# Performance work log

Hardware: AMD Instinct MI355X
Metric: run time of the kernel (lower is better)

The kernel has to match this reference:

```python
import jax, jax.numpy as jnp
import numpy as np

B, L, D_IN, D_OUT = 8, 2048, 256, 256


def setup_inputs() -> dict:
    key = jax.random.key(0)
    ks = jax.random.split(key, 7)
    s_in = 1.0 / np.sqrt(D_IN)
    return {
        "x": jax.random.normal(ks[0], (B, L, D_IN), dtype=jnp.float32),
        "Wq": jax.random.uniform(ks[1], (D_OUT, D_IN), jnp.float32, -s_in, s_in),
        "bq": jax.random.uniform(ks[2], (D_OUT,), jnp.float32, -s_in, s_in),
        "Wk": jax.random.uniform(ks[3], (D_OUT, D_IN), jnp.float32, -s_in, s_in),
        "bk": jax.random.uniform(ks[4], (D_OUT,), jnp.float32, -s_in, s_in),
        "Wv": jax.random.uniform(ks[5], (D_OUT, D_IN), jnp.float32, -s_in, s_in),
        "bv": jax.random.uniform(ks[6], (D_OUT,), jnp.float32, -s_in, s_in),
    }


def reference(x, Wq, bq, Wk, bk, Wv, bv):
    # QKV projections (torch Linear: y = x @ W.T + b)
    Q = jnp.einsum("bld,od->blo", x, Wq) + bq  # [B, L, D_OUT]
    K = jnp.einsum("bld,od->blo", x, Wk) + bk
    V = jnp.einsum("bld,od->blo", x, Wv) + bv
    scale = jnp.float32(D_OUT) ** 0.5
    E = jnp.einsum("bqd,bkd->bqk", Q, K) / scale  # [B, L, L]
    # NON-STANDARD: softmax over dim=1 (the query axis / columns of E)
    A = jax.nn.softmax(E, axis=1)
    C = jnp.einsum("bqk,bkd->bqd", A, V)  # [B, L, D_OUT]
    S_p = jnp.concatenate([Q, C], axis=1)  # [B, 2L, D_OUT]
    return (S_p, A)
```

## Files before the change

### kernel.cpp

```cpp
#include <hip/hip_runtime.h>
#include <hip/hip_bf16.h>
#include <stdint.h>

#define B_ 8
#define L_ 2048
#define D_ 256

typedef unsigned short u16;
typedef __attribute__((ext_vector_type(4))) float f32x4;
typedef __attribute__((ext_vector_type(8))) short bf16x8;

__device__ __forceinline__ u16 f2b(float f) {
  union { float f; unsigned u; } v; v.f = f;
  unsigned r = v.u + 0x7FFFu + ((v.u >> 16) & 1u);
  return (u16)(r >> 16);
}

__device__ __forceinline__ void comb(float& m, float& s, float m2, float s2) {
  float mn = fmaxf(m, m2);
  s = s * __expf(m - mn) + s2 * __expf(m2 - mn);
  m = mn;
}

__device__ __forceinline__ void async_copy16(const void* g, u16* l) {
  __builtin_amdgcn_global_load_lds(
      (const __attribute__((address_space(1))) unsigned*)g,
      (__attribute__((address_space(3))) unsigned*)l,
      16, 0, 0);
}

template<int KD>
__device__ __forceinline__ void gemm_core(const u16* __restrict__ Ag,
                                          const u16* __restrict__ Bg,
                                          int tile_m, int tile_n,
                                          u16* lds_a, u16* lds_b,
                                          f32x4 acc[4][4]) {
  const int tid  = threadIdx.x;
  const int wave = tid >> 6, lane = tid & 63;
  const int qd = lane >> 4, ln = lane & 15;
  const int wm = wave >> 1, wn = wave & 1;
  const int lrow = lane >> 2;
  const int lcol = (lane & 3) * 8;
  const u16* Abase = Ag + (size_t)tile_m * KD + lcol;
  const u16* Bbase = Bg + (size_t)tile_n * KD + lcol;

  for (int k0 = 0; k0 < KD; k0 += 32) {
#pragma unroll
    for (int j = 0; j < 2; ++j) {
      const int r0 = j * 64 + wave * 16;
      async_copy16(Abase + (size_t)(r0 + lrow) * KD + k0, lds_a + r0 * 32);
      async_copy16(Bbase + (size_t)(r0 + lrow) * KD + k0, lds_b + r0 * 32);
    }
    __syncthreads();
    bf16x8 af[4], bg[4];
#pragma unroll
    for (int i = 0; i < 4; ++i) {
      af[i] = *(const bf16x8*)(lds_a + (wm * 64 + i * 16 + ln) * 32 + qd * 8);
      bg[i] = *(const bf16x8*)(lds_b + (wn * 64 + i * 16 + ln) * 32 + qd * 8);
    }
#pragma unroll
    for (int i = 0; i < 4; ++i)
#pragma unroll
      for (int j = 0; j < 4; ++j)
        acc[i][j] = __builtin_amdgcn_mfma_f32_16x16x32_bf16(af[i], bg[j], acc[i][j], 0, 0, 0);
    __syncthreads();
  }
}

__global__ __launch_bounds__(256) void cvt_kernel(const float* __restrict__ x,
    const float* __restrict__ Wq, const float* __restrict__ Wk, const float* __restrict__ Wv,
    u16* __restrict__ xb, u16* __restrict__ Wb) {
  const int i = blockIdx.x * 256 + threadIdx.x;
  const int NX4 = (B_ * L_ * D_) / 4;
  f32x4 v;
  u16* dst;
  if (i < NX4) {
    v = ((const f32x4*)x)[i];
    dst = xb + (size_t)i * 4;
  } else {
    int wi = i - NX4;
    int z = wi >> 14;
    int off = wi & 16383;
    const float* W = (z == 0) ? Wq : (z == 1 ? Wk : Wv);
    v = ((const f32x4*)W)[off];
    dst = Wb + (size_t)z * 65536 + (size_t)off * 4;
  }
  unsigned p0 = (unsigned)f2b(v.x) | ((unsigned)f2b(v.y) << 16);
  unsigned p1 = (unsigned)f2b(v.z) | ((unsigned)f2b(v.w) << 16);
  *(uint2*)dst = make_uint2(p0, p1);
}

__global__ __launch_bounds__(256) void qkv_gemm(const u16* __restrict__ xb, const u16* __restrict__ Wb,
    const float* __restrict__ bq, const float* __restrict__ bk, const float* __restrict__ bv,
    u16* __restrict__ Qb, u16* __restrict__ Kb, u16* __restrict__ Vb,
    float* __restrict__ out_sp) {
  __shared__ u16 lds_a[128 * 32], lds_b[128 * 32];
  const int z = blockIdx.z;
  const float* bias = (z == 0) ? bq : (z == 1 ? bk : bv);
  u16* dst = (z == 0) ? Qb : (z == 1 ? Kb : Vb);
  const int tile_m = blockIdx.x * 128, tile_n = blockIdx.y * 128;
  f32x4 acc[4][4];
#pragma unroll
  for (int i = 0; i < 4; ++i)
#pragma unroll
    for (int j = 0; j < 4; ++j) acc[i][j] = (f32x4){0.f, 0.f, 0.f, 0.f};
  gemm_core<256>(xb, Wb + (size_t)z * 256 * 256, tile_m, tile_n, lds_a, lds_b, acc);

  const int lane = threadIdx.x & 63, wave = threadIdx.x >> 6;
  const int qd = lane >> 4, ln = lane & 15, wm = wave >> 1, wn = wave & 1;
#pragma unroll
  for (int i = 0; i < 4; ++i)
#pragma unroll
    for (int j = 0; j < 4; ++j) {
      const int col = tile_n + wn * 64 + j * 16 + ln;
      const float bvv = bias[col];
      const int row0 = tile_m + wm * 64 + i * 16 + qd * 4;
#pragma unroll
      for (int r = 0; r < 4; ++r) {
        const int row = row0 + r;
        const float val = acc[i][j][r] + bvv;
        dst[(size_t)row * D_ + col] = f2b(val);
        if (z == 0) {
          const int bb = row >> 11, l = row & 2047;
          out_sp[((size_t)bb * (2 * L_) + l) * D_ + col] = val;
        }
      }
    }
}

__global__ __launch_bounds__(256) void transpose_v(const u16* __restrict__ Vb, u16* __restrict__ Vbt) {
  const int b = blockIdx.z;
  const int l0 = blockIdx.x * 64;
  const int d0 = blockIdx.y * 64;
  __shared__ u16 t[64][65];
  const int tx = threadIdx.x & 63;
  const int ty = threadIdx.x >> 6;
  const u16* src = Vb + (size_t)b * L_ * D_;
  for (int j = ty; j < 64; j += 4)
    t[j][tx] = src[(size_t)(l0 + j) * D_ + d0 + tx];
  __syncthreads();
  u16* dst = Vbt + (size_t)b * D_ * L_;
  for (int j = ty; j < 64; j += 4)
    dst[(size_t)(d0 + j) * L_ + l0 + tx] = t[tx][j];
}

__global__ __launch_bounds__(256) void e_gemm(const u16* __restrict__ Qb, const u16* __restrict__ Kb,
                                              float* __restrict__ Ebuf,
                                              float* __restrict__ pm, float* __restrict__ ps) {
  __shared__ u16 lds_a[128 * 32], lds_b[128 * 32];
  __shared__ float sm_m[4][64], sm_s[4][64];
  const int b = blockIdx.z;
  const int tile_m = blockIdx.x * 128, tile_n = blockIdx.y * 128;
  f32x4 acc[4][4];
#pragma unroll
  for (int i = 0; i < 4; ++i)
#pragma unroll
    for (int j = 0; j < 4; ++j) acc[i][j] = (f32x4){0.f, 0.f, 0.f, 0.f};
  gemm_core<256>(Qb + (size_t)b * L_ * D_, Kb + (size_t)b * L_ * D_, tile_m, tile_n, lds_a, lds_b, acc);

  float* Eb = Ebuf + (size_t)b * L_ * L_;
  const int tid = threadIdx.x;
  const int lane = tid & 63, wave = tid >> 6;
  const int qd = lane >> 4, ln = lane & 15, wm = wave >> 1, wn = wave & 1;
#pragma unroll
  for (int j = 0; j < 4; ++j) {
    const int col = tile_n + wn * 64 + j * 16 + ln;
    const int row0 = tile_m + wm * 64 + qd * 4;
    float m = -1e30f;
#pragma unroll
    for (int i = 0; i < 4; ++i)
#pragma unroll
      for (int r = 0; r < 4; ++r)
        m = fmaxf(m, acc[i][j][r] * 0.0625f);
    float s = 0.f;
#pragma unroll
    for (int i = 0; i < 4; ++i)
#pragma unroll
      for (int r = 0; r < 4; ++r) {
        const float e = acc[i][j][r] * 0.0625f;
        Eb[(size_t)(row0 + i * 16 + r) * L_ + col] = e;
        s += __expf(e - m);
      }
    comb(m, s, __shfl_xor(m, 16), __shfl_xor(s, 16));
    comb(m, s, __shfl_xor(m, 32), __shfl_xor(s, 32));
    if (qd == 0) { sm_m[wave][j * 16 + ln] = m; sm_s[wave][j * 16 + ln] = s; }
  }
  __syncthreads();
  if (tid < 128) {
    const int w = tid >> 6, c = tid & 63;
    float m = sm_m[w][c], s = sm_s[w][c];
    comb(m, s, sm_m[w + 2][c], sm_s[w + 2][c]);
    const size_t idx = (size_t)blockIdx.x * (B_ * L_) + (size_t)b * L_ + tile_n + w * 64 + c;
    pm[idx] = m;
    ps[idx] = s;
  }
}

__global__ __launch_bounds__(256) void stats_reduce(const float* __restrict__ pm,
                                                    const float* __restrict__ ps,
                                                    float* __restrict__ mOut, float* __restrict__ rOut) {
  const int idx = blockIdx.x * 256 + threadIdx.x;
  float m = -1e30f, s = 0.f;
#pragma unroll
  for (int t = 0; t < 16; ++t)
    comb(m, s, pm[t * (B_ * L_) + idx], ps[t * (B_ * L_) + idx]);
  mOut[idx] = m;
  rOut[idx] = 1.0f / s;
}

__global__ __launch_bounds__(256) void apply_kernel(float* __restrict__ EA, u16* __restrict__ Ab,
                                                    const float* __restrict__ mArr,
                                                    const float* __restrict__ rArr) {
  const size_t i4 = (size_t)blockIdx.x * 256 + threadIdx.x;
  const int k4 = (int)(i4 & 511);
  const size_t row = i4 >> 9;
  const int b = (int)(row >> 11);
  f32x4 e = ((const f32x4*)EA)[i4];
  const f32x4 mv = *(const f32x4*)(mArr + (size_t)b * L_ + k4 * 4);
  const f32x4 rv = *(const f32x4*)(rArr + (size_t)b * L_ + k4 * 4);
  f32x4 a;
  a.x = __expf(e.x - mv.x) * rv.x;
  a.y = __expf(e.y - mv.y) * rv.y;
  a.z = __expf(e.z - mv.z) * rv.z;
  a.w = __expf(e.w - mv.w) * rv.w;
  ((f32x4*)EA)[i4] = a;
  unsigned p0 = (unsigned)f2b(a.x) | ((unsigned)f2b(a.y) << 16);
  unsigned p1 = (unsigned)f2b(a.z) | ((unsigned)f2b(a.w) << 16);
  *(uint2*)(Ab + i4 * 4) = make_uint2(p0, p1);
}

__global__ __launch_bounds__(256) void av_gemm(const u16* __restrict__ Ab, const u16* __restrict__ Vbt,
                                               float* __restrict__ out_sp) {
  __shared__ u16 lds_a[128 * 32], lds_b[128 * 32];
  const int b = blockIdx.z;
  const int tile_m = blockIdx.x * 128, tile_n = blockIdx.y * 128;
  f32x4 acc[4][4];
#pragma unroll
  for (int i = 0; i < 4; ++i)
#pragma unroll
    for (int j = 0; j < 4; ++j) acc[i][j] = (f32x4){0.f, 0.f, 0.f, 0.f};
  gemm_core<2048>(Ab + (size_t)b * L_ * L_, Vbt + (size_t)b * D_ * L_, tile_m, tile_n, lds_a, lds_b, acc);

  const int lane = threadIdx.x & 63, wave = threadIdx.x >> 6;
  const int qd = lane >> 4, ln = lane & 15, wm = wave >> 1, wn = wave & 1;
#pragma unroll
  for (int i = 0; i < 4; ++i)
#pragma unroll
    for (int j = 0; j < 4; ++j) {
      const int col = tile_n + wn * 64 + j * 16 + ln;
      const int row0 = tile_m + wm * 64 + i * 16 + qd * 4;
#pragma unroll
      for (int r = 0; r < 4; ++r)
        out_sp[((size_t)b * (2 * L_) + L_ + row0 + r) * D_ + col] = acc[i][j][r];
    }
}

extern "C" void kernel_launch(void* const* d_in, const int* in_sizes, int n_in,
                              void* d_out, int out_size, void* d_ws, size_t ws_size,
                              hipStream_t stream) {
  const float* x  = (const float*)d_in[0];
  const float* Wq = (const float*)d_in[1];
  const float* bq = (const float*)d_in[2];
  const float* Wk = (const float*)d_in[3];
  const float* bk = (const float*)d_in[4];
  const float* Wv = (const float*)d_in[5];
  const float* bv = (const float*)d_in[6];

  float* out    = (float*)d_out;
  float* outA   = out + (size_t)B_ * (2 * L_) * D_;

  u16* w   = (u16*)d_ws;
  u16* xb  = w;
  u16* Wb  = xb + 4194304;
  u16* Qb  = Wb + 196608;
  u16* Kb  = Qb + 4194304;
  u16* Vb  = Kb + 4194304;
  u16* Vbt = Vb + 4194304;
  u16* Ab  = Vbt + 4194304;
  float* mArr = (float*)(Ab + 33554432);
  float* rArr = mArr + B_ * L_;
  float* pm   = rArr + B_ * L_;
  float* ps   = pm + 16 * B_ * L_;

  cvt_kernel<<<4288, 256, 0, stream>>>(x, Wq, Wk, Wv, xb, Wb);
  qkv_gemm<<<dim3(128, 2, 3), 256, 0, stream>>>(xb, Wb, bq, bk, bv, Qb, Kb, Vb, out);
  transpose_v<<<dim3(32, 4, 8), 256, 0, stream>>>(Vb, Vbt);
  e_gemm<<<dim3(16, 16, 8), 256, 0, stream>>>(Qb, Kb, outA, pm, ps);
  stats_reduce<<<64, 256, 0, stream>>>(pm, ps, mArr, rArr);
  apply_kernel<<<32768, 256, 0, stream>>>(outA, Ab, mArr, rArr);
  av_gemm<<<dim3(16, 2, 8), 256, 0, stream>>>(Ab, Vbt, out);
}
```

Before: 325.3 us.

## Store logits as bf16 and fuse softmax apply into the AV GEMM

The E-GEMM now writes the scaled logits as bf16 into workspace instead of fp32 into the output A buffer. A new av_fused kernel reads those bf16 logits, applies exp/normalize with the column stats, writes fp32 A to the output, and feeds the bf16 probabilities directly through LDS into MFMA against V. This removes the separate apply pass and the Ab round trip, cutting HBM traffic on the large L×L matrices. In exchange, A is computed from bf16-rounded logits, which loses precision. The new GEMM also uses small 32-row tiles with no multi-stage pipelining and two barriers per k-step.

```diff
diff --git a/kernel.cpp b/kernel.cpp
--- a/kernel.cpp
+++ b/kernel.cpp
@@ -9,11 +9,16 @@
 typedef unsigned short u16;
 typedef __attribute__((ext_vector_type(4))) float f32x4;
 typedef __attribute__((ext_vector_type(8))) short bf16x8;
+typedef __attribute__((ext_vector_type(4))) short s16x4;
 
 __device__ __forceinline__ u16 f2b(float f) {
   union { float f; unsigned u; } v; v.f = f;
   unsigned r = v.u + 0x7FFFu + ((v.u >> 16) & 1u);
   return (u16)(r >> 16);
+}
+
+__device__ __forceinline__ float b2f(u16 h) {
+  union { unsigned u; float f; } v; v.u = (unsigned)h << 16; return v.f;
 }
 
 __device__ __forceinline__ void comb(float& m, float& s, float m2, float s2) {
@@ -145,7 +150,7 @@
 }
 
 __global__ __launch_bounds__(256) void e_gemm(const u16* __restrict__ Qb, const u16* __restrict__ Kb,
-                                              float* __restrict__ Ebuf,
+                                              u16* __restrict__ Eb16,
                                               float* __restrict__ pm, float* __restrict__ ps) {
   __shared__ u16 lds_a[128 * 32], lds_b[128 * 32];
   __shared__ float sm_m[4][64], sm_s[4][64];
@@ -158,7 +163,7 @@
     for (int j = 0; j < 4; ++j) acc[i][j] = (f32x4){0.f, 0.f, 0.f, 0.f};
   gemm_core<256>(Qb + (size_t)b * L_ * D_, Kb + (size_t)b * L_ * D_, tile_m, tile_n, lds_a, lds_b, acc);
 
-  float* Eb = Ebuf + (size_t)b * L_ * L_;
+  u16* Eb = Eb16 + (size_t)b * L_ * L_;
   const int tid = threadIdx.x;
   const int lane = tid & 63, wave = tid >> 6;
   const int qd = lane >> 4, ln = lane & 15, wm = wave >> 1, wn = wave & 1;
@@ -178,7 +183,7 @@
 #pragma unroll
       for (int r = 0; r < 4; ++r) {
         const float e = acc[i][j][r] * 0.0625f;
-        Eb[(size_t)(row0 + i * 16 + r) * L_ + col] = e;
+        Eb[(size_t)(row0 + i * 16 + r) * L_ + col] = f2b(e);
         s += __expf(e - m);
       }
     comb(m, s, __shfl_xor(m, 16), __shfl_xor(s, 16));
@@ -208,47 +213,73 @@
   rOut[idx] = 1.0f / s;
 }
 
-__global__ __launch_bounds__(256) void apply_kernel(float* __restrict__ EA, u16* __restrict__ Ab,
-                                                    const float* __restrict__ mArr,
-                                                    const float* __restrict__ rArr) {
-  const size_t i4 = (size_t)blockIdx.x * 256 + threadIdx.x;
-  const int k4 = (int)(i4 & 511);
-  const size_t row = i4 >> 9;
-  const int b = (int)(row >> 11);
-  f32x4 e = ((const f32x4*)EA)[i4];
-  const f32x4 mv = *(const f32x4*)(mArr + (size_t)b * L_ + k4 * 4);
-  const f32x4 rv = *(const f32x4*)(rArr + (size_t)b * L_ + k4 * 4);
-  f32x4 a;
-  a.x = __expf(e.x - mv.x) * rv.x;
-  a.y = __expf(e.y - mv.y) * rv.y;
-  a.z = __expf(e.z - mv.z) * rv.z;
-  a.w = __expf(e.w - mv.w) * rv.w;
-  ((f32x4*)EA)[i4] = a;
-  unsigned p0 = (unsigned)f2b(a.x) | ((unsigned)f2b(a.y) << 16);
-  unsigned p1 = (unsigned)f2b(a.z) | ((unsigned)f2b(a.w) << 16);
-  *(uint2*)(Ab + i4 * 4) = make_uint2(p0, p1);
-}
-
-__global__ __launch_bounds__(256) void av_gemm(const u16* __restrict__ Ab, const u16* __restrict__ Vbt,
-                                               float* __restrict__ out_sp) {
-  __shared__ u16 lds_a[128 * 32], lds_b[128 * 32];
-  const int b = blockIdx.z;
-  const int tile_m = blockIdx.x * 128, tile_n = blockIdx.y * 128;
-  f32x4 acc[4][4];
-#pragma unroll
-  for (int i = 0; i < 4; ++i)
+__global__ __launch_bounds__(256) void av_fused(const u16* __restrict__ Eb16, const u16* __restrict__ Vbt,
+                                                const float* __restrict__ mArr, const float* __restrict__ rArr,
+                                                float* __restrict__ Aout, float* __restrict__ out_sp) {
+  __shared__ u16 lds_b[256 * 32];
+  __shared__ u16 lds_a[32 * 32];
+  const int b = blockIdx.y;
+  const int tile_m = blockIdx.x * 32;
+  const int tid = threadIdx.x;
+  const int wave = tid >> 6, lane = tid & 63;
+  const int qd = lane >> 4, ln = lane & 15;
+  const int lrow = lane >> 2, lcol = (lane & 3) * 8;
+
+  const u16* Vb_ = Vbt + (size_t)b * D_ * L_ + lcol;
+  const int arow = tid >> 3, koff = (tid & 7) * 4;
+  const u16* Erow = Eb16 + ((size_t)b * L_ + tile_m + arow) * L_ + koff;
+  float* Arow = Aout + ((size_t)(b * L_ + tile_m + arow)) * L_ + koff;
+  const float* mrow = mArr + (size_t)b * L_ + koff;
+  const float* rrow = rArr + (size_t)b * L_ + koff;
+
+  f32x4 acc[2][4];
+#pragma unroll
+  for (int i = 0; i < 2; ++i)
 #pragma unroll
     for (int j = 0; j < 4; ++j) acc[i][j] = (f32x4){0.f, 0.f, 0.f, 0.f};
-  gemm_core<2048>(Ab + (size_t)b * L_ * L_, Vbt + (size_t)b * D_ * L_, tile_m, tile_n, lds_a, lds_b, acc);
-
-  const int lane = threadIdx.x & 63, wave = threadIdx.x >> 6;
-  const int qd = lane >> 4, ln = lane & 15, wm = wave >> 1, wn = wave & 1;
-#pragma unroll
-  for (int i = 0; i < 4; ++i)
+
+  for (int k0 = 0; k0 < L_; k0 += 32) {
+#pragma unroll
+    for (int jj = 0; jj < 4; ++jj) {
+      const int r0 = wave * 64 + jj * 16;
+      async_copy16(Vb_ + (size_t)(r0 + lrow) * L_ + k0, lds_b + r0 * 32);
+    }
+    s16x4 ev = *(const s16x4*)(Erow + k0);
+    const f32x4 mv = *(const f32x4*)(mrow + k0);
+    const f32x4 rv = *(const f32x4*)(rrow + k0);
+    f32x4 a;
+    a.x = __expf(b2f((u16)ev.x) - mv.x) * rv.x;
+    a.y = __expf(b2f((u16)ev.y) - mv.y) * rv.y;
+    a.z = __expf(b2f((u16)ev.z) - mv.z) * rv.z;
+    a.w = __expf(b2f((u16)ev.w) - mv.w) * rv.w;
+    *(f32x4*)(Arow + k0) = a;
+    uint2 pk;
+    pk.x = (unsigned)f2b(a.x) | ((unsigned)f2b(a.y) << 16);
+    pk.y = (unsigned)f2b(a.z) | ((unsigned)f2b(a.w) << 16);
+    *(uint2*)(lds_a + (size_t)tid * 4) = pk;
+    __syncthreads();
+
+    bf16x8 af[2], bg[4];
+#pragma unroll
+    for (int i = 0; i < 2; ++i)
+      af[i] = *(const bf16x8*)(lds_a + (i * 16 + ln) * 32 + qd * 8);
+#pragma unroll
+    for (int j = 0; j < 4; ++j)
+      bg[j] = *(const bf16x8*)(lds_b + (wave * 64 + j * 16 + ln) * 32 + qd * 8);
+#pragma unroll
+    for (int i = 0; i < 2; ++i)
+#pragma unroll
+      for (int j = 0; j < 4; ++j)
+        acc[i][j] = __builtin_amdgcn_mfma_f32_16x16x32_bf16(af[i], bg[j], acc[i][j], 0, 0, 0);
+    __syncthreads();
+  }
+
+#pragma unroll
+  for (int i = 0; i < 2; ++i)
 #pragma unroll
     for (int j = 0; j < 4; ++j) {
-      const int col = tile_n + wn * 64 + j * 16 + ln;
-      const int row0 = tile_m + wm * 64 + i * 16 + qd * 4;
+      const int col = wave * 64 + j * 16 + ln;
+      const int row0 = tile_m + i * 16 + qd * 4;
 #pragma unroll
       for (int r = 0; r < 4; ++r)
         out_sp[((size_t)b * (2 * L_) + L_ + row0 + r) * D_ + col] = acc[i][j][r];
@@ -269,15 +300,15 @@
   float* out    = (float*)d_out;
   float* outA   = out + (size_t)B_ * (2 * L_) * D_;
 
-  u16* w   = (u16*)d_ws;
-  u16* xb  = w;
-  u16* Wb  = xb + 4194304;
-  u16* Qb  = Wb + 196608;
-  u16* Kb  = Qb + 4194304;
-  u16* Vb  = Kb + 4194304;
-  u16* Vbt = Vb + 4194304;
-  u16* Ab  = Vbt + 4194304;
-  float* mArr = (float*)(Ab + 33554432);
+  u16* w    = (u16*)d_ws;
+  u16* xb   = w;
+  u16* Wb   = xb + 4194304;
+  u16* Qb   = Wb + 196608;
+  u16* Kb   = Qb + 4194304;
+  u16* Vb   = Kb + 4194304;
+  u16* Vbt  = Vb + 4194304;
+  u16* Eb16 = Vbt + 4194304;
+  float* mArr = (float*)(Eb16 + 33554432);
   float* rArr = mArr + B_ * L_;
   float* pm   = rArr + B_ * L_;
   float* ps   = pm + 16 * B_ * L_;
@@ -285,8 +316,7 @@
   cvt_kernel<<<4288, 256, 0, stream>>>(x, Wq, Wk, Wv, xb, Wb);
   qkv_gemm<<<dim3(128, 2, 3), 256, 0, stream>>>(xb, Wb, bq, bk, bv, Qb, Kb, Vb, out);
   transpose_v<<<dim3(32, 4, 8), 256, 0, stream>>>(Vb, Vbt);
-  e_gemm<<<dim3(16, 16, 8), 256, 0, stream>>>(Qb, Kb, outA, pm, ps);
+  e_gemm<<<dim3(16, 16, 8), 256, 0, stream>>>(Qb, Kb, Eb16, pm, ps);
   stats_reduce<<<64, 256, 0, stream>>>(pm, ps, mArr, rArr);
-  apply_kernel<<<32768, 256, 0, stream>>>(outA, Ab, mArr, rArr);
-  av_gemm<<<dim3(16, 2, 8), 256, 0, stream>>>(Ab, Vbt, out);
-}
+  av_fused<<<dim3(64, 8), 256, 0, stream>>>(Eb16, Vbt, mArr, rArr, outA, out);
+}
```

Result: no change. 319.1 us (-1.9%).
